# Performance work log

Measured on AMD Instinct MI355X. Metric: run time of the kernel, lower is better.

The kernel has to match this reference:

```python
import jax, jax.numpy as jnp
import numpy as np

N0 = 131072
K = 7
NODES = [N0, N0 // 2, N0 // 4, N0 // 8]      # nodes at each of the 4 levels
NEXT = [N0 // 2, N0 // 4, N0 // 8, N0 // 16]  # kept nodes after each level (M=0.5)
HID = 80
EPS = 1e-5


def _bn(x, g, b):
    # BatchNorm1d, training-mode stats over nodes (biased variance, eps=1e-5)
    m = x.mean(axis=0)
    v = ((x - m) ** 2).mean(axis=0)
    return (x - m) * jax.lax.rsqrt(v + EPS) * g + b


def setup_inputs() -> dict:
    key = jax.random.key(0)
    ks = jax.random.split(key, 16)
    inp = {}
    inp["feat"] = jax.random.normal(ks[0], (N0, 6), dtype=jnp.float32)
    inp["bn1_g"] = jnp.ones((6,), jnp.float32)
    inp["bn1_b"] = jnp.zeros((6,), jnp.float32)
    inp["W_emb"] = jax.random.normal(ks[1], (6, HID), jnp.float32) / np.sqrt(6.0)
    inp["embn_g"] = jnp.ones((HID,), jnp.float32)
    inp["embn_b"] = jnp.zeros((HID,), jnp.float32)
    inp["W_msg"] = jax.random.normal(ks[2], (4, HID, HID), jnp.float32) / np.sqrt(HID)
    inp["W1"] = jax.random.normal(ks[3], (HID, 64), jnp.float32) / np.sqrt(HID)
    inp["b1"] = jnp.zeros((64,), jnp.float32)
    inp["W2"] = jax.random.normal(ks[4], (64, 64), jnp.float32) / 8.0
    inp["b2"] = jnp.zeros((64,), jnp.float32)
    inp["W3"] = jax.random.normal(ks[5], (64, 64), jnp.float32) / 8.0
    inp["b3"] = jnp.zeros((64,), jnp.float32)
    inp["bn2_g"] = jnp.ones((64,), jnp.float32)
    inp["bn2_b"] = jnp.zeros((64,), jnp.float32)
    inp["Wc"] = jax.random.normal(ks[6], (64, 13), jnp.float32) / 8.0
    # KNN edge lists per level (k=7 neighbors per node), precomputed indices
    for l in range(4):
        n = NODES[l]
        e = K * n
        inp[f"i{l}"] = jax.random.randint(ks[7 + 2 * l], (e,), 0, n, dtype=jnp.int32)
        inp[f"j{l}"] = jax.random.randint(ks[8 + 2 * l], (e,), 0, n, dtype=jnp.int32)
    # kept-node (upsample-anchor) indices per level: unique, deterministic
    for l in range(4):
        inp[f"up{l}"] = jnp.arange(NEXT[l], dtype=jnp.int32)
    return inp


def _forward(feat, bn1_g, bn1_b, W_emb, embn_g, embn_b, W_msg,
             W1, b1, W2, b2, W3, b3, bn2_g, bn2_b, Wc, edges, ups):
    h = _bn(feat, bn1_g, bn1_b)
    h = jax.nn.relu(_bn(h @ W_emb, embn_g, embn_b))
    full_up, ij_pairs, latest = [], [], []
    h_up_down = h
    for l in range(4):
        i, j = edges[l]
        n = h.shape[0]
        # Swin3D block: gather neighbor feats, transform, scatter-sum, residual ELU
        msg = h[j] @ W_msg[l]                               # [E_l, HID]
        agg = jax.ops.segment_sum(msg, i, num_segments=n)   # [N_l, HID]
        features = jax.nn.elu(h + agg)
        ij_pairs.append((i, j))
        full_up.append(ups[l])
        h = features[ups[l]]                                # downsample (M=0.5)
        fd = features
        ii, jj = i, j
        for it in range(l + 1):
            # push_info_down: copy_u + sum along edges (src=j, dst=i)
            hud = jax.ops.segment_sum(fd[jj], ii, num_segments=fd.shape[0])
            if l - it < len(latest):
                latest[l - it] = hud
            else:
                latest.append(hud)
            if l >= 1 and l - it - 1 >= 0:
                prev = latest[l - it - 1].at[full_up[l - it - 1]].set(hud)
                latest[l - it - 1] = prev
                fd = prev
                ii, jj = ij_pairs[l - it - 1]
            h_up_down = hud
    x = jax.nn.elu(h_up_down @ W1 + b1)
    x = jax.nn.elu(x @ W2 + b2)
    x = jax.nn.elu(x @ W3 + b3)
    x = _bn(x, bn2_g, bn2_b)
    return x @ Wc  # [N0, 13]


def reference(feat, bn1_g, bn1_b, W_emb, embn_g, embn_b, W_msg,
              W1, b1, W2, b2, W3, b3, bn2_g, bn2_b, Wc,
              i0, j0, i1, j1, i2, j2, i3, j3, up0, up1, up2, up3):
    edges = [(i0, j0), (i1, j1), (i2, j2), (i3, j3)]
    ups = [up0, up1, up2, up3]
    return _forward(feat, bn1_g, bn1_b, W_emb, embn_g, embn_b, W_msg,
                    W1, b1, W2, b2, W3, b3, bn2_g, bn2_b, Wc, edges, ups)
```

## Files before the change

kernel.cpp:

```cpp
#include <hip/hip_runtime.h>
#include <math.h>


#define HID 80
constexpr int cN0 = 131072;

__device__ __forceinline__ float eluf(float x) { return x > 0.f ? x : expm1f(x); }

__global__ void k_bn1_stats(const float* __restrict__ feat, float* __restrict__ pacc) {
  float s[6] = {0,0,0,0,0,0}, q[6] = {0,0,0,0,0,0};
  int idx = blockIdx.x * blockDim.x + threadIdx.x;
  int stride = gridDim.x * blockDim.x;
  for (int r2 = idx; r2 < cN0 / 2; r2 += stride) {
    const float4* p = (const float4*)(feat + (size_t)r2 * 12);
    float4 a = p[0], b = p[1], c = p[2];
    s[0] += a.x + b.z;  q[0] += a.x*a.x + b.z*b.z;
    s[1] += a.y + b.w;  q[1] += a.y*a.y + b.w*b.w;
    s[2] += a.z + c.x;  q[2] += a.z*a.z + c.x*c.x;
    s[3] += a.w + c.y;  q[3] += a.w*a.w + c.y*c.y;
    s[4] += b.x + c.z;  q[4] += b.x*b.x + c.z*c.z;
    s[5] += b.y + c.w;  q[5] += b.y*b.y + c.w*c.w;
  }
#pragma unroll
  for (int k = 0; k < 6; k++) {
    for (int off = 32; off; off >>= 1) {
      s[k] += __shfl_down(s[k], off, 64);
      q[k] += __shfl_down(q[k], off, 64);
    }
  }
  __shared__ float ls[4][12];
  int wid = threadIdx.x >> 6;
  if ((threadIdx.x & 63) == 0) {
#pragma unroll
    for (int k = 0; k < 6; k++) { ls[wid][k] = s[k]; ls[wid][6 + k] = q[k]; }
  }
  __syncthreads();
  if (threadIdx.x < 12) {
    pacc[blockIdx.x * 12 + threadIdx.x] =
        ls[0][threadIdx.x] + ls[1][threadIdx.x] + ls[2][threadIdx.x] + ls[3][threadIdx.x];
  }
}

__global__ void k_finalize(const float* __restrict__ pacc, int npart,
                           const float* __restrict__ g, const float* __restrict__ b,
                           float* __restrict__ ss, int ncols, float inv_n) {
  extern __shared__ float red[];
  int C2 = 2 * ncols;
  int t = threadIdx.x;
  int c2 = t % C2;
  int sub = t / C2;
  int nsub = blockDim.x / C2;
  float s = 0.f;
  if (sub < nsub)
    for (int p = sub; p < npart; p += nsub) s += pacc[p * C2 + c2];
  if (t < C2) red[t] = 0.f;
  __syncthreads();
  if (sub < nsub) atomicAdd(&red[c2], s);
  __syncthreads();
  if (t < ncols) {
    float m = red[t] * inv_n;
    float v = red[ncols + t] * inv_n - m * m;
    float sc = g[t] * rsqrtf(v + 1e-5f);
    ss[t] = sc;
    ss[ncols + t] = b[t] - m * sc;
  }
}

__global__ void k_emb4(const float* __restrict__ feat, const float* __restrict__ Wemb,
                       const float* __restrict__ ss, float* __restrict__ t) {
  __shared__ float Wl[6 * HID];
  __shared__ float sc[12];
  for (int i = threadIdx.x; i < 6 * HID; i += blockDim.x) Wl[i] = Wemb[i];
  if (threadIdx.x < 12) sc[threadIdx.x] = ss[threadIdx.x];
  __syncthreads();
  int gid = blockIdx.x * blockDim.x + threadIdx.x;
  if (gid >= cN0 * (HID/4)) return;
  int r = gid / (HID/4);
  int c4 = (gid - r * (HID/4)) * 4;
  float a[6];
#pragma unroll
  for (int k = 0; k < 6; k++) a[k] = feat[r*6 + k] * sc[k] + sc[6 + k];
  float4 o;
  float* op = (float*)&o;
#pragma unroll
  for (int i = 0; i < 4; i++) {
    float v = 0.f;
#pragma unroll
    for (int k = 0; k < 6; k++) v += a[k] * Wl[k*HID + c4 + i];
    op[i] = v;
  }
  *(float4*)(t + (size_t)r*HID + c4) = o;
}

__global__ void k_colstats(const float* __restrict__ x, int nrows, int ncols,
                           float* __restrict__ pacc) {
  extern __shared__ float ls[];
  int c = threadIdx.x % ncols;
  int sub = threadIdx.x / ncols;
  int rows_per = blockDim.x / ncols;
  for (int i = threadIdx.x; i < 2*ncols; i += blockDim.x) ls[i] = 0.f;
  __syncthreads();
  float s = 0.f, q = 0.f;
  for (int r = blockIdx.x * rows_per + sub; r < nrows; r += gridDim.x * rows_per) {
    float v = x[(size_t)r * ncols + c];
    s += v; q += v*v;
  }
  atomicAdd(&ls[c], s);
  atomicAdd(&ls[ncols + c], q);
  __syncthreads();
  for (int i = threadIdx.x; i < 2*ncols; i += blockDim.x)
    pacc[blockIdx.x * 2 * ncols + i] = ls[i];
}

__global__ void k_scale_relu4(float* __restrict__ x, const float* __restrict__ ss, int ntot4) {
  int gid = blockIdx.x * blockDim.x + threadIdx.x;
  if (gid >= ntot4) return;
  int r = gid / (HID/4);
  int c4 = (gid - r * (HID/4)) * 4;
  float4 t = *(float4*)(x + (size_t)r*HID + c4);
  float* tp = (float*)&t;
#pragma unroll
  for (int i = 0; i < 4; i++) {
    float v = tp[i] * ss[c4 + i] + ss[HID + c4 + i];
    tp[i] = v > 0.f ? v : 0.f;
  }
  *(float4*)(x + (size_t)r*HID + c4) = t;
}

#define NBINS 240
#define NEDGE_TOT 1720320
#define BIN_CHUNK 2048
#define NWG 840

struct BinP {
  const int* ii[4]; const int* jj[4];
  int* hist;
  int* offs;
  int* total;
  int* base;
  int* pairs;
  int* rp[4]; int* col[4];
};

__device__ __forceinline__ int edge_level(int gid, int& el) {
  if (gid < 917504)  { el = gid;           return 0; }
  if (gid < 1376256) { el = gid - 917504;  return 1; }
  if (gid < 1605632) { el = gid - 1376256; return 2; }
  el = gid - 1605632; return 3;
}
__device__ __forceinline__ int blk_level(int b, int& lb) {
  if (b < 128) { lb = b;       return 0; }
  if (b < 192) { lb = b - 128; return 1; }
  if (b < 224) { lb = b - 192; return 2; }
  lb = b - 224; return 3;
}
__constant__ const int cNN[4] = {131072, 65536, 32768, 16384};
__constant__ const int cNE[4] = {917504, 458752, 229376, 114688};
__constant__ const int cNB[4] = {128, 64, 32, 16};
__constant__ const int cLB[4] = {0, 128, 192, 224};

__global__ void k_binA(BinP p) {
  __shared__ int h[NBINS];
  for (int i = threadIdx.x; i < NBINS; i += 256) h[i] = 0;
  __syncthreads();
  int ebase = blockIdx.x * BIN_CHUNK;
#pragma unroll
  for (int it = 0; it < BIN_CHUNK / 256; it++) {
    int e = ebase + it * 256 + threadIdx.x;
    int el; int l = edge_level(e, el);
    atomicAdd(&h[cLB[l] + (p.ii[l][el] >> 10)], 1);
  }
  __syncthreads();
  for (int b = threadIdx.x; b < NBINS; b += 256)
    p.hist[blockIdx.x * NBINS + b] = h[b];
}

__global__ void k_binT(BinP p) {
  __shared__ int sd[256];
  int b = blockIdx.x;
  int t = threadIdx.x;
  int carry = 0;
  for (int r = 0; r < 4; r++) {
    int idx = r * 256 + t;
    int v = (idx < NWG) ? p.hist[idx * NBINS + b] : 0;
    sd[t] = v;
    __syncthreads();
    for (int off = 1; off < 256; off <<= 1) {
      int x = sd[t];
      if (t >= off) x += sd[t - off];
      __syncthreads();
      sd[t] = x;
      __syncthreads();
    }
    if (idx < NWG) p.offs[b * NWG + idx] = carry + sd[t] - v;
    carry += sd[255];
    __syncthreads();
  }
  if (t == 0) p.total[b] = carry;
}

__global__ void k_binScan2(BinP p) {
  __shared__ int sd[256];
  int t = threadIdx.x;
  int v = (t < NBINS) ? p.total[t] : 0;
  sd[t] = v;
  __syncthreads();
  for (int off = 1; off < 256; off <<= 1) {
    int x = sd[t];
    if (t >= off) x += sd[t - off];
    __syncthreads();
    sd[t] = x;
    __syncthreads();
  }
  if (t < NBINS) p.base[t] = sd[t] - v;
  if (t == NBINS - 1) p.base[NBINS] = sd[t];
}

__global__ void k_binB(BinP p) {
  __shared__ int cur[NBINS];
  int wg = blockIdx.x;
  for (int b = threadIdx.x; b < NBINS; b += 256)
    cur[b] = p.base[b] + p.offs[b * NWG + wg];
  __syncthreads();
  int ebase = wg * BIN_CHUNK;
#pragma unroll
  for (int it = 0; it < BIN_CHUNK / 256; it++) {
    int e = ebase + it * 256 + threadIdx.x;
    int el; int l = edge_level(e, el);
    int i = p.ii[l][el], j = p.jj[l][el];
    int b = cLB[l] + (i >> 10);
    int gpos = atomicAdd(&cur[b], 1);
    p.pairs[gpos] = ((i & 1023) << 17) | j;
  }
}

__global__ void __launch_bounds__(256) k_binCSR(BinP p) {
  __shared__ int d[1024];
  __shared__ int sd[256];
  int lb; int l = blk_level(blockIdx.x, lb);
  int t = threadIdx.x;
  int e0g = p.base[blockIdx.x];
  int e1g = p.base[blockIdx.x + 1];
  int lvlbase = p.base[cLB[l]];
  int e0 = e0g - lvlbase;
  for (int i = t; i < 1024; i += 256) d[i] = 0;
  __syncthreads();
  for (int e = e0g + t; e < e1g; e += 256)
    atomicAdd(&d[p.pairs[e] >> 17], 1);
  __syncthreads();
  int a0 = d[4*t], a1 = d[4*t+1], a2 = d[4*t+2], a3 = d[4*t+3];
  int ts = a0 + a1 + a2 + a3;
  sd[t] = ts;
  __syncthreads();
  for (int off = 1; off < 256; off <<= 1) {
    int x = sd[t];
    if (t >= off) x += sd[t - off];
    __syncthreads();
    sd[t] = x;
    __syncthreads();
  }
  int c0 = e0 + sd[t] - ts;
  int c1 = c0 + a0, c2 = c1 + a1, c3 = c2 + a2;
  int* rp = p.rp[l];
  *(int4*)(rp + lb * 1024 + 4 * t) = make_int4(c0, c1, c2, c3);
  if (t == 0 && lb == cNB[l] - 1) rp[cNN[l]] = cNE[l];
  d[4*t] = c0; d[4*t+1] = c1; d[4*t+2] = c2; d[4*t+3] = c3;
  __syncthreads();
  int* col = p.col[l];
  for (int e = e0g + t; e < e1g; e += 256) {
    int pk = p.pairs[e];
    int slot = atomicAdd(&d[pk >> 17], 1);
    col[slot] = pk & 0x1FFFF;
  }
}

template <int KIN, int KOUT, bool ELU>
__global__ void __launch_bounds__(256) k_gemm(const float* __restrict__ in,
                                              const float* __restrict__ W,
                                              const float* __restrict__ bias,
                                              float* __restrict__ out) {
  constexpr int CPT = KOUT / 4;
  __shared__ float As[KIN * 64];
  int rbase = blockIdx.x * 64;
  for (int idx = threadIdx.x; idx < 16 * KIN; idx += 256) {
    int r = idx / (KIN / 4);
    int q = idx - r * (KIN / 4);
    float4 v = *(const float4*)(in + (size_t)(rbase + r) * KIN + q * 4);
    As[(q * 4 + 0) * 64 + r] = v.x;
    As[(q * 4 + 1) * 64 + r] = v.y;
    As[(q * 4 + 2) * 64 + r] = v.z;
    As[(q * 4 + 3) * 64 + r] = v.w;
  }
  __syncthreads();
  int row = threadIdx.x & 63;
  int c0 = __builtin_amdgcn_readfirstlane((threadIdx.x >> 6) * CPT);
  float acc[CPT];
#pragma unroll
  for (int i = 0; i < CPT; i++) acc[i] = bias ? bias[c0 + i] : 0.f;
#pragma unroll 4
  for (int k = 0; k < KIN; k++) {
    float a = As[k * 64 + row];
    const float* wk = W + (size_t)k * KOUT + c0;
#pragma unroll
    for (int i = 0; i < CPT; i++) acc[i] += a * wk[i];
  }
  float* orow = out + (size_t)(rbase + row) * KOUT + c0;
#pragma unroll
  for (int u = 0; u < CPT / 4; u++) {
    float v0 = acc[4*u+0], v1 = acc[4*u+1], v2 = acc[4*u+2], v3 = acc[4*u+3];
    if (ELU) {
      v0 = v0 > 0.f ? v0 : expm1f(v0);  v1 = v1 > 0.f ? v1 : expm1f(v1);
      v2 = v2 > 0.f ? v2 : expm1f(v2);  v3 = v3 > 0.f ? v3 : expm1f(v3);
    }
    float4 o; o.x = v0; o.y = v1; o.z = v2; o.w = v3;
    *(float4*)(orow + 4 * u) = o;
  }
}

__global__ void k_agg_elu4(const float* __restrict__ h, const float* __restrict__ hW,
                           const int* __restrict__ rp, const int* __restrict__ col,
                           float* __restrict__ f, int n) {
  int gid = blockIdx.x * blockDim.x + threadIdx.x;
  if (gid >= n * (HID/4)) return;
  int v = gid / (HID/4);
  int c4 = (gid - v * (HID/4)) * 4;
  int e0 = rp[v], e1 = rp[v + 1];
  float4 s = *(const float4*)(h + (size_t)v*HID + c4);
  float* sp = (float*)&s;
  for (int e = e0; e < e1; e++) {
    int j = col[e];
    float4 x = *(const float4*)(hW + (size_t)j*HID + c4);
    sp[0] += x.x; sp[1] += x.y; sp[2] += x.z; sp[3] += x.w;
  }
#pragma unroll
  for (int i = 0; i < 4; i++) sp[i] = eluf(sp[i]);
  *(float4*)(f + (size_t)v*HID + c4) = s;
}

__global__ void k_prop4(const float* __restrict__ top, const float* __restrict__ oldb,
                        int half, const int* __restrict__ rp, const int* __restrict__ col,
                        float* __restrict__ dst, int n) {
  int gid = blockIdx.x * blockDim.x + threadIdx.x;
  if (gid >= n * (HID/4)) return;
  int v = gid / (HID/4);
  int c4 = (gid - v * (HID/4)) * 4;
  int e0 = rp[v], e1 = rp[v + 1];
  float4 s = {0,0,0,0};
  float* sp = (float*)&s;
  for (int e = e0; e < e1; e++) {
    int j = col[e];
    const float* src = (j < half) ? top : oldb;
    float4 x = *(const float4*)(src + (size_t)j*HID + c4);
    sp[0] += x.x; sp[1] += x.y; sp[2] += x.z; sp[3] += x.w;
  }
  *(float4*)(dst + (size_t)v*HID + c4) = s;
}

__global__ void k_fin_bn2(const float* __restrict__ pacc, int npart,
                          const float* __restrict__ g, const float* __restrict__ b,
                          const float* __restrict__ Wc, float* __restrict__ wcp) {
  __shared__ float red[128];
  __shared__ float sc[64], sh[64];
  int t = threadIdx.x;
  int c2 = t & 127;
  int sub = t >> 7;
  float s = 0.f;
  for (int p = sub; p < npart; p += 8) s += pacc[p * 128 + c2];
  if (t < 128) red[t] = 0.f;
  __syncthreads();
  atomicAdd(&red[c2], s);
  __syncthreads();
  if (t < 64) {
    float invn = 1.f / (float)cN0;
    float m = red[t] * invn;
    float v = red[64 + t] * invn - m * m;
    float scv = g[t] * rsqrtf(v + 1e-5f);
    sc[t] = scv;
    sh[t] = b[t] - m * scv;
  }
  __syncthreads();
  for (int i = t; i < 64 * 13; i += 1024) { int c = i / 13; wcp[i] = sc[c] * Wc[i]; }
  if (t < 13) {
    float acc13 = 0.f;
    for (int c = 0; c < 64; c++) acc13 += sh[c] * Wc[c*13 + t];
    wcp[64*13 + t] = acc13;
  }
}

__global__ void k_final(const float* __restrict__ x3, const float* __restrict__ wcp,
                        float* __restrict__ out) {
  __shared__ float Wl[64*13 + 13];
  for (int i = threadIdx.x; i < 64*13 + 13; i += blockDim.x) Wl[i] = wcp[i];
  __syncthreads();
  int gid = blockIdx.x * blockDim.x + threadIdx.x;
  int r = gid / 13, o = gid - r * 13;
  const float* row = x3 + (size_t)r * 64;
  float s = Wl[64*13 + o];
#pragma unroll
  for (int c = 0; c < 64; c++) s += row[c] * Wl[c*13 + o];
  out[gid] = s;
}

extern "C" void kernel_launch(void* const* d_in, const int* in_sizes, int n_in,
                              void* d_out, int out_size, void* d_ws, size_t ws_size,
                              hipStream_t stream) {
  const float* feat   = (const float*)d_in[0];
  const float* bn1_g  = (const float*)d_in[1];
  const float* bn1_b  = (const float*)d_in[2];
  const float* W_emb  = (const float*)d_in[3];
  const float* embn_g = (const float*)d_in[4];
  const float* embn_b = (const float*)d_in[5];
  const float* W_msg  = (const float*)d_in[6];
  const float* W1 = (const float*)d_in[7];
  const float* b1 = (const float*)d_in[8];
  const float* W2 = (const float*)d_in[9];
  const float* b2 = (const float*)d_in[10];
  const float* W3 = (const float*)d_in[11];
  const float* b3 = (const float*)d_in[12];
  const float* bn2_g = (const float*)d_in[13];
  const float* bn2_b = (const float*)d_in[14];
  const float* Wc    = (const float*)d_in[15];

  const int NNODE[4] = {131072, 65536, 32768, 16384};
  const int NEDGE[4] = {917504, 458752, 229376, 114688};
  const int N = cN0;
  const int SBLK = 256;
  const int BN1B = 64;

  size_t off = 0;
  char* base = (char*)d_ws;
  auto af = [&](size_t nf) -> float* { float* p = (float*)(base + off); off += ((nf*4 + 255) & ~(size_t)255); return p; };
  auto ai = [&](size_t ni) -> int*   { int*   p = (int*)  (base + off); off += ((ni*4 + 255) & ~(size_t)255); return p; };

  int* hist   = ai((size_t)NWG * NBINS);
  int* offs   = ai((size_t)NBINS * NWG);
  int* total  = ai(NBINS);
  int* bbase  = ai(NBINS + 1);
  int* pairs  = ai(NEDGE_TOT);

  float* pacc1 = af((size_t)BN1B * 12);
  float* pacce = af((size_t)SBLK * 160);
  float* pacc2 = af((size_t)SBLK * 128);
  float* ss1 = af(12);
  float* sse = af(160);
  float* wcp = af(64*13 + 13);
  int* rp[4];   for (int l = 0; l < 4; l++) rp[l]   = ai(NNODE[l] + 1);
  int* col[4];  for (int l = 0; l < 4; l++) col[l]  = ai(NEDGE[l]);

  float* t_h0 = af((size_t)N * HID);
  float* hWb  = af((size_t)N * HID);
  float* f[4];
  f[0] = af((size_t)NNODE[0] * HID);
  f[1] = af((size_t)NNODE[1] * HID);
  f[2] = af((size_t)NNODE[2] * HID);
  f[3] = af((size_t)NNODE[3] * HID);
  float* h1a = af((size_t)NNODE[1] * HID);
  float* h1b = af((size_t)NNODE[1] * HID);
  float* h2a = af((size_t)NNODE[2] * HID);
  float* h2b = af((size_t)NNODE[2] * HID);
  float* h3  = af((size_t)NNODE[3] * HID);

  float* x1 = f[0];
  float* x2 = f[1];
  float* x3 = f[0];
  (void)ws_size; (void)in_sizes; (void)n_in; (void)out_size;

  k_bn1_stats<<<BN1B, 256, 0, stream>>>(feat, pacc1);
  k_finalize<<<1, 1024, 2*6*4, stream>>>(pacc1, BN1B, bn1_g, bn1_b, ss1, 6, 1.f / N);
  k_emb4<<<(N * (HID/4)) / 256, 256, 0, stream>>>(feat, W_emb, ss1, t_h0);
  k_colstats<<<SBLK, 320, 2*80*4, stream>>>(t_h0, N, 80, pacce);
  k_finalize<<<1, 1024, 2*80*4, stream>>>(pacce, SBLK, embn_g, embn_b, sse, 80, 1.f / N);
  k_scale_relu4<<<(N * (HID/4)) / 256, 256, 0, stream>>>(t_h0, sse, N * (HID/4));

  BinP bp;
  for (int l = 0; l < 4; l++) {
    bp.ii[l] = (const int*)d_in[16 + 2*l];
    bp.jj[l] = (const int*)d_in[17 + 2*l];
    bp.rp[l] = rp[l]; bp.col[l] = col[l];
  }
  bp.hist = hist; bp.offs = offs; bp.total = total; bp.base = bbase; bp.pairs = pairs;
  k_binA<<<NWG, 256, 0, stream>>>(bp);
  k_binT<<<NBINS, 256, 0, stream>>>(bp);
  k_binScan2<<<1, 256, 0, stream>>>(bp);
  k_binB<<<NWG, 256, 0, stream>>>(bp);
  k_binCSR<<<NBINS, 256, 0, stream>>>(bp);

  const float* hin = t_h0;
  for (int l = 0; l < 4; l++) {
    int n = NNODE[l];
    k_gemm<80, 80, false><<<n / 64, 256, 0, stream>>>(hin, W_msg + (size_t)l * HID * HID, nullptr, hWb);
    k_agg_elu4<<<(n * (HID/4)) / 256, 256, 0, stream>>>(hin, hWb, rp[l], col[l], f[l], n);
    hin = f[l];
  }

  float* H0P = t_h0;
  float* H0Q = hWb;
  const int B = 256;
  k_prop4<<<(NNODE[0]*(HID/4))/B, B, 0, stream>>>(f[0], f[0], NNODE[0], rp[0], col[0], H0P, NNODE[0]);
  k_prop4<<<(NNODE[1]*(HID/4))/B, B, 0, stream>>>(f[1], f[1], NNODE[1], rp[1], col[1], h1a, NNODE[1]);
  k_prop4<<<(NNODE[0]*(HID/4))/B, B, 0, stream>>>(h1a, H0P, 65536, rp[0], col[0], H0Q, NNODE[0]);
  k_prop4<<<(NNODE[2]*(HID/4))/B, B, 0, stream>>>(f[2], f[2], NNODE[2], rp[2], col[2], h2a, NNODE[2]);
  k_prop4<<<(NNODE[1]*(HID/4))/B, B, 0, stream>>>(h2a, h1a, 32768, rp[1], col[1], h1b, NNODE[1]);
  k_prop4<<<(NNODE[0]*(HID/4))/B, B, 0, stream>>>(h1b, H0Q, 65536, rp[0], col[0], H0P, NNODE[0]);
  k_prop4<<<(NNODE[3]*(HID/4))/B, B, 0, stream>>>(f[3], f[3], NNODE[3], rp[3], col[3], h3, NNODE[3]);
  k_prop4<<<(NNODE[2]*(HID/4))/B, B, 0, stream>>>(h3, h2a, 16384, rp[2], col[2], h2b, NNODE[2]);
  k_prop4<<<(NNODE[1]*(HID/4))/B, B, 0, stream>>>(h2b, h1b, 32768, rp[1], col[1], h1a, NNODE[1]);
  k_prop4<<<(NNODE[0]*(HID/4))/B, B, 0, stream>>>(h1a, H0P, 65536, rp[0], col[0], H0Q, NNODE[0]);

  k_gemm<80, 64, true><<<N / 64, 256, 0, stream>>>(H0Q, W1, b1, x1);
  k_gemm<64, 64, true><<<N / 64, 256, 0, stream>>>(x1, W2, b2, x2);
  k_gemm<64, 64, true><<<N / 64, 256, 0, stream>>>(x2, W3, b3, x3);
  k_colstats<<<SBLK, 256, 2*64*4, stream>>>(x3, N, 64, pacc2);
  k_fin_bn2<<<1, 1024, 0, stream>>>(pacc2, SBLK, bn2_g, bn2_b, Wc, wcp);
  k_final<<<(N * 13) / 256, 256, 0, stream>>>(x3, wcp, (float*)d_out);
}
```

Baseline: 929.3 us.

## Fold both embedding batchnorms analytically and batch independent propagation passes

Computes the feature covariance in the first statistics pass, then derives the embedding batchnorm's per-column variance analytically from W_emb. Both normalizations fold into one affine weight and bias, which removes the column-stats pass, a finalize kernel and the separate scale+ReLU pass over the N×80 activation. Independent push-down propagation launches are also grouped into four multi-job launches by dependency wave, cutting launch count and filling the GPU during the small-level passes. The covariance-based variance can differ slightly in rounding from the direct two-pass computation.

```diff
diff --git a/kernel.cpp b/kernel.cpp
--- a/kernel.cpp
+++ b/kernel.cpp
@@ -9,17 +9,28 @@
 
 __global__ void k_bn1_stats(const float* __restrict__ feat, float* __restrict__ pacc) {
   float s[6] = {0,0,0,0,0,0}, q[6] = {0,0,0,0,0,0};
+  float cp[15] = {0,0,0,0,0,0,0,0,0,0,0,0,0,0,0};
   int idx = blockIdx.x * blockDim.x + threadIdx.x;
   int stride = gridDim.x * blockDim.x;
   for (int r2 = idx; r2 < cN0 / 2; r2 += stride) {
     const float4* p = (const float4*)(feat + (size_t)r2 * 12);
     float4 a = p[0], b = p[1], c = p[2];
-    s[0] += a.x + b.z;  q[0] += a.x*a.x + b.z*b.z;
-    s[1] += a.y + b.w;  q[1] += a.y*a.y + b.w*b.w;
-    s[2] += a.z + c.x;  q[2] += a.z*a.z + c.x*c.x;
-    s[3] += a.w + c.y;  q[3] += a.w*a.w + c.y*c.y;
-    s[4] += b.x + c.z;  q[4] += b.x*b.x + c.z*c.z;
-    s[5] += b.y + c.w;  q[5] += b.y*b.y + c.w*c.w;
+    float f0[6], f1[6];
+    f0[0]=a.x; f0[1]=a.y; f0[2]=a.z; f0[3]=a.w; f0[4]=b.x; f0[5]=b.y;
+    f1[0]=b.z; f1[1]=b.w; f1[2]=c.x; f1[3]=c.y; f1[4]=c.z; f1[5]=c.w;
+#pragma unroll
+    for (int k = 0; k < 6; k++) {
+      s[k] += f0[k] + f1[k];
+      q[k] += f0[k]*f0[k] + f1[k]*f1[k];
+    }
+    int ci = 0;
+#pragma unroll
+    for (int k = 0; k < 6; k++)
+#pragma unroll
+      for (int k2 = k + 1; k2 < 6; k2++) {
+        cp[ci] += f0[k]*f0[k2] + f1[k]*f1[k2];
+        ci++;
+      }
   }
 #pragma unroll
   for (int k = 0; k < 6; k++) {
@@ -28,50 +39,84 @@
       q[k] += __shfl_down(q[k], off, 64);
     }
   }
-  __shared__ float ls[4][12];
+#pragma unroll
+  for (int k = 0; k < 15; k++) {
+    for (int off = 32; off; off >>= 1) cp[k] += __shfl_down(cp[k], off, 64);
+  }
+  __shared__ float ls[4][27];
   int wid = threadIdx.x >> 6;
   if ((threadIdx.x & 63) == 0) {
 #pragma unroll
     for (int k = 0; k < 6; k++) { ls[wid][k] = s[k]; ls[wid][6 + k] = q[k]; }
-  }
-  __syncthreads();
-  if (threadIdx.x < 12) {
-    pacc[blockIdx.x * 12 + threadIdx.x] =
+#pragma unroll
+    for (int k = 0; k < 15; k++) ls[wid][12 + k] = cp[k];
+  }
+  __syncthreads();
+  if (threadIdx.x < 27) {
+    pacc[blockIdx.x * 27 + threadIdx.x] =
         ls[0][threadIdx.x] + ls[1][threadIdx.x] + ls[2][threadIdx.x] + ls[3][threadIdx.x];
   }
 }
 
-__global__ void k_finalize(const float* __restrict__ pacc, int npart,
-                           const float* __restrict__ g, const float* __restrict__ b,
-                           float* __restrict__ ss, int ncols, float inv_n) {
-  extern __shared__ float red[];
-  int C2 = 2 * ncols;
+__global__ void k_fold(const float* __restrict__ pacc, int npart,
+                       const float* __restrict__ g1, const float* __restrict__ eg,
+                       const float* __restrict__ eb, const float* __restrict__ Wemb,
+                       float* __restrict__ fw) {
+  __shared__ float mom[27];
+  __shared__ float m6[6], grs[6];
+  __shared__ float Ch[6][6];
   int t = threadIdx.x;
-  int c2 = t % C2;
-  int sub = t / C2;
-  int nsub = blockDim.x / C2;
-  float s = 0.f;
-  if (sub < nsub)
-    for (int p = sub; p < npart; p += nsub) s += pacc[p * C2 + c2];
-  if (t < C2) red[t] = 0.f;
-  __syncthreads();
-  if (sub < nsub) atomicAdd(&red[c2], s);
-  __syncthreads();
-  if (t < ncols) {
-    float m = red[t] * inv_n;
-    float v = red[ncols + t] * inv_n - m * m;
-    float sc = g[t] * rsqrtf(v + 1e-5f);
-    ss[t] = sc;
-    ss[ncols + t] = b[t] - m * sc;
-  }
-}
-
-__global__ void k_emb4(const float* __restrict__ feat, const float* __restrict__ Wemb,
-                       const float* __restrict__ ss, float* __restrict__ t) {
+  if (t < 27) {
+    float s = 0.f;
+    for (int p = 0; p < npart; p++) s += pacc[p * 27 + t];
+    mom[t] = s;
+  }
+  __syncthreads();
+  const float invn = 1.f / (float)cN0;
+  if (t < 6) {
+    float m = mom[t] * invn;
+    float v = mom[6 + t] * invn - m * m;
+    m6[t] = m;
+    grs[t] = g1[t] * rsqrtf(v + 1e-5f);
+  }
+  __syncthreads();
+  if (t < 36) {
+    int k = t / 6, k2 = t % 6;
+    float S;
+    if (k == k2) S = mom[6 + k];
+    else {
+      int a = k < k2 ? k : k2, b = k < k2 ? k2 : k;
+      int idx = 12 + 5 * a - (a * (a - 1)) / 2 + (b - a - 1);
+      S = mom[idx];
+    }
+    Ch[k][k2] = (S * invn - m6[k] * m6[k2]) * grs[k] * grs[k2];
+  }
+  __syncthreads();
+  for (int c = t; c < HID; c += blockDim.x) {
+    float w[6];
+#pragma unroll
+    for (int k = 0; k < 6; k++) w[k] = Wemb[k * HID + c];
+    float var = 0.f;
+#pragma unroll
+    for (int k = 0; k < 6; k++)
+#pragma unroll
+      for (int k2 = 0; k2 < 6; k2++) var += w[k] * w[k2] * Ch[k][k2];
+    float A = eg[c] * rsqrtf(var + 1e-5f);
+    float dot = 0.f;
+#pragma unroll
+    for (int k = 0; k < 6; k++) dot += grs[k] * m6[k] * w[k];
+#pragma unroll
+    for (int k = 0; k < 6; k++) fw[k * HID + c] = grs[k] * A * w[k];
+    fw[6 * HID + c] = eb[c] - A * dot;
+  }
+}
+
+__global__ void k_emb4(const float* __restrict__ feat, const float* __restrict__ fw,
+                       float* __restrict__ h) {
   __shared__ float Wl[6 * HID];
-  __shared__ float sc[12];
-  for (int i = threadIdx.x; i < 6 * HID; i += blockDim.x) Wl[i] = Wemb[i];
-  if (threadIdx.x < 12) sc[threadIdx.x] = ss[threadIdx.x];
+  __shared__ float bl[HID];
+  for (int i = threadIdx.x; i < 6 * HID; i += blockDim.x) Wl[i] = fw[i];
+  if (threadIdx.x < HID) bl[threadIdx.x] = fw[6 * HID + threadIdx.x];
   __syncthreads();
   int gid = blockIdx.x * blockDim.x + threadIdx.x;
   if (gid >= cN0 * (HID/4)) return;
@@ -79,17 +124,17 @@
   int c4 = (gid - r * (HID/4)) * 4;
   float a[6];
 #pragma unroll
-  for (int k = 0; k < 6; k++) a[k] = feat[r*6 + k] * sc[k] + sc[6 + k];
+  for (int k = 0; k < 6; k++) a[k] = feat[r*6 + k];
   float4 o;
   float* op = (float*)&o;
 #pragma unroll
   for (int i = 0; i < 4; i++) {
-    float v = 0.f;
+    float v = bl[c4 + i];
 #pragma unroll
     for (int k = 0; k < 6; k++) v += a[k] * Wl[k*HID + c4 + i];
-    op[i] = v;
-  }
-  *(float4*)(t + (size_t)r*HID + c4) = o;
+    op[i] = v > 0.f ? v : 0.f;
+  }
+  *(float4*)(h + (size_t)r*HID + c4) = o;
 }
 
 __global__ void k_colstats(const float* __restrict__ x, int nrows, int ncols,
@@ -112,21 +157,6 @@
     pacc[blockIdx.x * 2 * ncols + i] = ls[i];
 }
 
-__global__ void k_scale_relu4(float* __restrict__ x, const float* __restrict__ ss, int ntot4) {
-  int gid = blockIdx.x * blockDim.x + threadIdx.x;
-  if (gid >= ntot4) return;
-  int r = gid / (HID/4);
-  int c4 = (gid - r * (HID/4)) * 4;
-  float4 t = *(float4*)(x + (size_t)r*HID + c4);
-  float* tp = (float*)&t;
-#pragma unroll
-  for (int i = 0; i < 4; i++) {
-    float v = tp[i] * ss[c4 + i] + ss[HID + c4 + i];
-    tp[i] = v > 0.f ? v : 0.f;
-  }
-  *(float4*)(x + (size_t)r*HID + c4) = t;
-}
-
 #define NBINS 240
 #define NEDGE_TOT 1720320
 #define BIN_CHUNK 2048
@@ -134,11 +164,7 @@
 
 struct BinP {
   const int* ii[4]; const int* jj[4];
-  int* hist;
-  int* offs;
-  int* total;
-  int* base;
-  int* pairs;
+  int* hist; int* offs; int* total; int* base; int* pairs;
   int* rp[4]; int* col[4];
 };
 
@@ -337,13 +363,32 @@
   *(float4*)(f + (size_t)v*HID + c4) = s;
 }
 
-__global__ void k_prop4(const float* __restrict__ top, const float* __restrict__ oldb,
-                        int half, const int* __restrict__ rp, const int* __restrict__ col,
-                        float* __restrict__ dst, int n) {
-  int gid = blockIdx.x * blockDim.x + threadIdx.x;
+struct PropJobs {
+  const float* top[4]; const float* oldb[4];
+  const int* rp[4]; const int* col[4];
+  int half[4]; int n[4];
+  int cum[4];
+  float* dst[4];
+  int njobs;
+};
+
+__global__ void k_prop_multi(PropJobs J) {
+  int b = blockIdx.x;
+  int g = 0;
+  if (J.njobs > 1 && b >= J.cum[0]) g = 1;
+  if (J.njobs > 2 && b >= J.cum[1]) g = 2;
+  if (J.njobs > 3 && b >= J.cum[2]) g = 3;
+  int lb = g ? (b - J.cum[g - 1]) : b;
+  int gid = lb * 256 + (int)threadIdx.x;
+  int n = J.n[g];
   if (gid >= n * (HID/4)) return;
   int v = gid / (HID/4);
   int c4 = (gid - v * (HID/4)) * 4;
+  const int* rp = J.rp[g];
+  const int* col = J.col[g];
+  const float* top = J.top[g];
+  const float* oldb = J.oldb[g];
+  int half = J.half[g];
   int e0 = rp[v], e1 = rp[v + 1];
   float4 s = {0,0,0,0};
   float* sp = (float*)&s;
@@ -353,7 +398,7 @@
     float4 x = *(const float4*)(src + (size_t)j*HID + c4);
     sp[0] += x.x; sp[1] += x.y; sp[2] += x.z; sp[3] += x.w;
   }
-  *(float4*)(dst + (size_t)v*HID + c4) = s;
+  *(float4*)(J.dst[g] + (size_t)v*HID + c4) = s;
 }
 
 __global__ void k_fin_bn2(const float* __restrict__ pacc, int npart,
@@ -406,7 +451,6 @@
                               hipStream_t stream) {
   const float* feat   = (const float*)d_in[0];
   const float* bn1_g  = (const float*)d_in[1];
-  const float* bn1_b  = (const float*)d_in[2];
   const float* W_emb  = (const float*)d_in[3];
   const float* embn_g = (const float*)d_in[4];
   const float* embn_b = (const float*)d_in[5];
@@ -438,11 +482,9 @@
   int* bbase  = ai(NBINS + 1);
   int* pairs  = ai(NEDGE_TOT);
 
-  float* pacc1 = af((size_t)BN1B * 12);
-  float* pacce = af((size_t)SBLK * 160);
+  float* pacc1 = af((size_t)BN1B * 27);
   float* pacc2 = af((size_t)SBLK * 128);
-  float* ss1 = af(12);
-  float* sse = af(160);
+  float* fw  = af(6*HID + HID);
   float* wcp = af(64*13 + 13);
   int* rp[4];   for (int l = 0; l < 4; l++) rp[l]   = ai(NNODE[l] + 1);
   int* col[4];  for (int l = 0; l < 4; l++) col[l]  = ai(NEDGE[l]);
@@ -466,11 +508,8 @@
   (void)ws_size; (void)in_sizes; (void)n_in; (void)out_size;
 
   k_bn1_stats<<<BN1B, 256, 0, stream>>>(feat, pacc1);
-  k_finalize<<<1, 1024, 2*6*4, stream>>>(pacc1, BN1B, bn1_g, bn1_b, ss1, 6, 1.f / N);
-  k_emb4<<<(N * (HID/4)) / 256, 256, 0, stream>>>(feat, W_emb, ss1, t_h0);
-  k_colstats<<<SBLK, 320, 2*80*4, stream>>>(t_h0, N, 80, pacce);
-  k_finalize<<<1, 1024, 2*80*4, stream>>>(pacce, SBLK, embn_g, embn_b, sse, 80, 1.f / N);
-  k_scale_relu4<<<(N * (HID/4)) / 256, 256, 0, stream>>>(t_h0, sse, N * (HID/4));
+  k_fold<<<1, 256, 0, stream>>>(pacc1, BN1B, bn1_g, embn_g, embn_b, W_emb, fw);
+  k_emb4<<<(N * (HID/4)) / 256, 256, 0, stream>>>(feat, fw, t_h0);
 
   BinP bp;
   for (int l = 0; l < 4; l++) {
@@ -495,17 +534,37 @@
 
   float* H0P = t_h0;
   float* H0Q = hWb;
-  const int B = 256;
-  k_prop4<<<(NNODE[0]*(HID/4))/B, B, 0, stream>>>(f[0], f[0], NNODE[0], rp[0], col[0], H0P, NNODE[0]);
-  k_prop4<<<(NNODE[1]*(HID/4))/B, B, 0, stream>>>(f[1], f[1], NNODE[1], rp[1], col[1], h1a, NNODE[1]);
-  k_prop4<<<(NNODE[0]*(HID/4))/B, B, 0, stream>>>(h1a, H0P, 65536, rp[0], col[0], H0Q, NNODE[0]);
-  k_prop4<<<(NNODE[2]*(HID/4))/B, B, 0, stream>>>(f[2], f[2], NNODE[2], rp[2], col[2], h2a, NNODE[2]);
-  k_prop4<<<(NNODE[1]*(HID/4))/B, B, 0, stream>>>(h2a, h1a, 32768, rp[1], col[1], h1b, NNODE[1]);
-  k_prop4<<<(NNODE[0]*(HID/4))/B, B, 0, stream>>>(h1b, H0Q, 65536, rp[0], col[0], H0P, NNODE[0]);
-  k_prop4<<<(NNODE[3]*(HID/4))/B, B, 0, stream>>>(f[3], f[3], NNODE[3], rp[3], col[3], h3, NNODE[3]);
-  k_prop4<<<(NNODE[2]*(HID/4))/B, B, 0, stream>>>(h3, h2a, 16384, rp[2], col[2], h2b, NNODE[2]);
-  k_prop4<<<(NNODE[1]*(HID/4))/B, B, 0, stream>>>(h2b, h1b, 32768, rp[1], col[1], h1a, NNODE[1]);
-  k_prop4<<<(NNODE[0]*(HID/4))/B, B, 0, stream>>>(h1a, H0P, 65536, rp[0], col[0], H0Q, NNODE[0]);
+  auto nb = [](int n) { return (n * (HID/4)) / 256; };
+
+  PropJobs g1{};
+  g1.njobs = 4;
+  g1.top[0]=f[0]; g1.oldb[0]=f[0]; g1.half[0]=NNODE[0]; g1.rp[0]=rp[0]; g1.col[0]=col[0]; g1.dst[0]=H0P; g1.n[0]=NNODE[0];
+  g1.top[1]=f[1]; g1.oldb[1]=f[1]; g1.half[1]=NNODE[1]; g1.rp[1]=rp[1]; g1.col[1]=col[1]; g1.dst[1]=h1a; g1.n[1]=NNODE[1];
+  g1.top[2]=f[2]; g1.oldb[2]=f[2]; g1.half[2]=NNODE[2]; g1.rp[2]=rp[2]; g1.col[2]=col[2]; g1.dst[2]=h2a; g1.n[2]=NNODE[2];
+  g1.top[3]=f[3]; g1.oldb[3]=f[3]; g1.half[3]=NNODE[3]; g1.rp[3]=rp[3]; g1.col[3]=col[3]; g1.dst[3]=h3;  g1.n[3]=NNODE[3];
+  g1.cum[0]=nb(NNODE[0]); g1.cum[1]=g1.cum[0]+nb(NNODE[1]); g1.cum[2]=g1.cum[1]+nb(NNODE[2]); g1.cum[3]=g1.cum[2]+nb(NNODE[3]);
+  k_prop_multi<<<g1.cum[3], 256, 0, stream>>>(g1);
+
+  PropJobs g2{};
+  g2.njobs = 3;
+  g2.top[0]=h1a; g2.oldb[0]=H0P; g2.half[0]=65536; g2.rp[0]=rp[0]; g2.col[0]=col[0]; g2.dst[0]=H0Q; g2.n[0]=NNODE[0];
+  g2.top[1]=h2a; g2.oldb[1]=h1a; g2.half[1]=32768; g2.rp[1]=rp[1]; g2.col[1]=col[1]; g2.dst[1]=h1b; g2.n[1]=NNODE[1];
+  g2.top[2]=h3;  g2.oldb[2]=h2a; g2.half[2]=16384; g2.rp[2]=rp[2]; g2.col[2]=col[2]; g2.dst[2]=h2b; g2.n[2]=NNODE[2];
+  g2.cum[0]=nb(NNODE[0]); g2.cum[1]=g2.cum[0]+nb(NNODE[1]); g2.cum[2]=g2.cum[1]+nb(NNODE[2]);
+  k_prop_multi<<<g2.cum[2], 256, 0, stream>>>(g2);
+
+  PropJobs g3{};
+  g3.njobs = 2;
+  g3.top[0]=h1b; g3.oldb[0]=H0Q; g3.half[0]=65536; g3.rp[0]=rp[0]; g3.col[0]=col[0]; g3.dst[0]=H0P; g3.n[0]=NNODE[0];
+  g3.top[1]=h2b; g3.oldb[1]=h1b; g3.half[1]=32768; g3.rp[1]=rp[1]; g3.col[1]=col[1]; g3.dst[1]=h1a; g3.n[1]=NNODE[1];
+  g3.cum[0]=nb(NNODE[0]); g3.cum[1]=g3.cum[0]+nb(NNODE[1]);
+  k_prop_multi<<<g3.cum[1], 256, 0, stream>>>(g3);
+
+  PropJobs g4{};
+  g4.njobs = 1;
+  g4.top[0]=h1a; g4.oldb[0]=H0P; g4.half[0]=65536; g4.rp[0]=rp[0]; g4.col[0]=col[0]; g4.dst[0]=H0Q; g4.n[0]=NNODE[0];
+  g4.cum[0]=nb(NNODE[0]);
+  k_prop_multi<<<g4.cum[0], 256, 0, stream>>>(g4);
 
   k_gemm<80, 64, true><<<N / 64, 256, 0, stream>>>(H0Q, W1, b1, x1);
   k_gemm<64, 64, true><<<N / 64, 256, 0, stream>>>(x1, W2, b2, x2);
```

After: 807.5 us, median of 2. 13.1% less time.
